# Kernel optimization log

Hardware: AMD Instinct MI355X
Metric: run time of the kernel (lower is better)

Reference implementation:

```python
import jax, jax.numpy as jnp
import numpy as np

N, IN, H1, H2, E, NE = 32768, 768, 2048, 1024, 64, 256
K_PAIRS, T_TRIP = 4096, 8192
TEMP, MARGIN, BETA = 0.1, 0.2, 0.001


def setup_inputs() -> dict:
    key = jax.random.key(0)
    ks = jax.random.split(key, 18)

    def w(k, i, o):
        return (jax.random.normal(k, (i, o), jnp.float32) / np.sqrt(i)).astype(jnp.float32)

    return {
        'x': jax.random.normal(ks[0], (N, IN), jnp.float32),
        'q_embs': jax.random.normal(ks[1], (N, IN), jnp.float32),
        'qd_align_w': jax.random.uniform(ks[2], (N,), jnp.float32),
        'pairs': jax.random.randint(ks[3], (K_PAIRS, 2), 0, N, jnp.int32),
        'triplets': jax.random.randint(ks[4], (T_TRIP, 3), 0, N, jnp.int32),
        'enc_w0': w(ks[5], IN, H1), 'enc_b0': jnp.zeros((H1,), jnp.float32),
        'enc_w1': w(ks[6], H1, H2), 'enc_b1': jnp.zeros((H2,), jnp.float32),
        'enc_w2': w(ks[7], H2, E), 'enc_b2': jnp.zeros((E,), jnp.float32),
        'dec_w0': w(ks[8], E, H2), 'dec_b0': jnp.zeros((H2,), jnp.float32),
        'dec_w1': w(ks[9], H2, H1), 'dec_b1': jnp.zeros((H1,), jnp.float32),
        'dec_w2': w(ks[10], H1, IN), 'dec_b2': jnp.zeros((IN,), jnp.float32),
        'codebook': w(ks[11], NE, E),
    }


def _mlp(h, w0, b0, w1, b1, w2, b2):
    h = jax.nn.relu(h @ w0 + b0)
    h = jax.nn.relu(h @ w1 + b1)
    return h @ w2 + b2


def _vqvae_forward(x, q_embs, qd_align_w, pairs, triplets,
                   enc_w0, enc_b0, enc_w1, enc_b1, enc_w2, enc_b2,
                   dec_w0, dec_b0, dec_w1, dec_b1, dec_w2, dec_b2, codebook):
    sg = jax.lax.stop_gradient
    # encoder on items and queries
    z = _mlp(x, enc_w0, enc_b0, enc_w1, enc_b1, enc_w2, enc_b2)            # [N, E]
    qz = _mlp(q_embs, enc_w0, enc_b0, enc_w1, enc_b1, enc_w2, enc_b2)      # [N, E]
    # vector quantize: nearest codebook entry
    d = (jnp.sum(z * z, axis=1, keepdims=True)
         - 2.0 * (z @ codebook.T)
         + jnp.sum(codebook * codebook, axis=1))                           # [N, NE]
    idx = jnp.argmin(d, axis=1)                                            # [N]
    x_q = codebook[idx]                                                    # [N, E]
    vq_loss = jnp.mean((x_q - sg(z)) ** 2) + BETA * jnp.mean((sg(x_q) - z) ** 2)
    x_q_st = z + sg(x_q - z)                                               # straight-through
    out = _mlp(x_q_st, dec_w0, dec_b0, dec_w1, dec_b1, dec_w2, dec_b2)     # [N, IN]
    # qd align: weighted cosine similarity between item and query encodings
    cos = jnp.sum(z * qz, axis=-1) / jnp.maximum(
        jnp.linalg.norm(z, axis=-1) * jnp.linalg.norm(qz, axis=-1), 1e-8)
    qd_align_loss = 1.0 - jnp.mean(qd_align_w * cos)
    # outer contrastive (InfoNCE over all rows; pos col replaces itself so
    # CE over [pos, all-but-pos] == logsumexp(all) - pos)
    xn = x_q_st / jnp.maximum(jnp.linalg.norm(x_q_st, axis=1, keepdims=True), 1e-12)
    sim = (xn[pairs[:, 0]] @ xn.T) / TEMP                                  # [K, N]
    pos = jnp.take_along_axis(sim, pairs[:, 1:2].astype(jnp.int32), axis=1)[:, 0]
    outer_con_loss = jnp.mean(jax.nn.logsumexp(sim, axis=1) - pos)
    # inner triplet loss on encoder features
    a, p, n = z[triplets[:, 0]], z[triplets[:, 1]], z[triplets[:, 2]]
    dp = jnp.sqrt(jnp.sum((a - p) ** 2, axis=-1) + 1e-12)
    dn = jnp.sqrt(jnp.sum((a - n) ** 2, axis=-1) + 1e-12)
    inner_triplet_loss = jnp.mean(jax.nn.relu(dp - dn + MARGIN))
    return out, vq_loss, idx[:, None], x_q_st, outer_con_loss, inner_triplet_loss, qd_align_loss


def reference(x, q_embs, qd_align_w, pairs, triplets,
              enc_w0, enc_b0, enc_w1, enc_b1, enc_w2, enc_b2,
              dec_w0, dec_b0, dec_w1, dec_b1, dec_w2, dec_b2, codebook):
    return _vqvae_forward(x, q_embs, qd_align_w, pairs, triplets,
                          enc_w0, enc_b0, enc_w1, enc_b1, enc_w2, enc_b2,
                          dec_w0, dec_b0, dec_w1, dec_b1, dec_w2, dec_b2, codebook)
```

## Files before the change

kernel.cpp:

```cpp
#include <hip/hip_runtime.h>
#include <hip/hip_bf16.h>

namespace {
constexpr int kN = 32768, kIN = 768, kH1 = 2048, kH2 = 1024, kE = 64, kNE = 256;
constexpr int kKP = 4096, kTT = 8192;
constexpr int kCh = 4096;
constexpr int kMaxFix = 4096;

constexpr size_t OFF_OUT = 0;
constexpr size_t OFF_VQ  = (size_t)kN * kIN;
constexpr size_t OFF_IDX = OFF_VQ + 1;
constexpr size_t OFF_XQ  = OFF_IDX + (size_t)kN;
constexpr size_t OFF_OCL = OFF_XQ + (size_t)kN * kE;
constexpr size_t OFF_ITL = OFF_OCL + 1;
constexpr size_t OFF_QDA = OFF_ITL + 1;
}

typedef short bf16x8 __attribute__((ext_vector_type(8)));
typedef float f32x4 __attribute__((ext_vector_type(4)));

__device__ __forceinline__ unsigned short f2bf(float v) {
  __hip_bfloat16 h = __float2bfloat16(v);
  return *reinterpret_cast<unsigned short*>(&h);
}
__device__ __forceinline__ float bf2f(unsigned short u) {
  __hip_bfloat16 h = *reinterpret_cast<__hip_bfloat16*>(&u);
  return __bfloat162float(h);
}

__device__ __forceinline__ void gload_lds16(const void* g, void* lds) {
  __builtin_amdgcn_global_load_lds(
      (const __attribute__((address_space(1))) void*)g,
      (__attribute__((address_space(3))) void*)lds, 16, 0, 0);
}

template <int BM, int BN, int BK, bool RELU, bool OUTF, bool OUTB>
__global__ __launch_bounds__(256) void gemm_bt(const unsigned short* __restrict__ A,
                                               const unsigned short* __restrict__ Bt,
                                               const float* __restrict__ bias,
                                               float* __restrict__ Cf,
                                               unsigned short* __restrict__ Cb,
                                               int N, int K) {
  constexpr int WM = BM / 2, WN = BN / 2, TMt = WM / 16, TNt = WN / 16;
  constexpr int CH = BK / 8;
  constexpr int RA = BM * BK / 2048, RB = BN * BK / 2048;
  __shared__ unsigned short As[BM * BK];
  __shared__ unsigned short Bs[BN * BK];
  const int tid = threadIdx.x, lane = tid & 63, wave = tid >> 6;
  const int wm = (wave >> 1) * WM, wn = (wave & 1) * WN;
  const int l15 = lane & 15, quad = lane >> 4;
  const int rowA0 = blockIdx.y * BM, colB0 = blockIdx.x * BN;
  f32x4 acc[TMt][TNt];
#pragma unroll
  for (int i = 0; i < TMt; ++i)
#pragma unroll
    for (int j = 0; j < TNt; ++j) acc[i][j] = (f32x4){0.f, 0.f, 0.f, 0.f};

  const char* Ab = (const char*)A;
  const char* Bb = (const char*)Bt;
  char* AsB = (char*)As;
  char* BsB = (char*)Bs;

  for (int k0 = 0; k0 < K; k0 += BK) {
    if (k0) __syncthreads();
#pragma unroll
    for (int r = 0; r < RA; ++r) {
      int off = (r * 256 + tid) * 16;
      int row = off / (BK * 2);
      int sc = ((off >> 4) ^ row) & (CH - 1);
      gload_lds16(Ab + (size_t)(rowA0 + row) * (K * 2) + (size_t)k0 * 2 + sc * 16,
                  AsB + off);
    }
#pragma unroll
    for (int r = 0; r < RB; ++r) {
      int off = (r * 256 + tid) * 16;
      int row = off / (BK * 2);
      int sc = ((off >> 4) ^ row) & (CH - 1);
      gload_lds16(Bb + (size_t)(colB0 + row) * (K * 2) + (size_t)k0 * 2 + sc * 16,
                  BsB + off);
    }
    __syncthreads();
#pragma unroll
    for (int ks = 0; ks < BK; ks += 32) {
      bf16x8 af[TMt], bfr[TNt];
#pragma unroll
      for (int i = 0; i < TMt; ++i) {
        int row = wm + i * 16 + l15;
        int c = (((ks >> 3) + quad) ^ row) & (CH - 1);
        af[i] = *(const bf16x8*)(AsB + row * (BK * 2) + c * 16);
      }
#pragma unroll
      for (int j = 0; j < TNt; ++j) {
        int col = wn + j * 16 + l15;
        int c = (((ks >> 3) + quad) ^ col) & (CH - 1);
        bfr[j] = *(const bf16x8*)(BsB + col * (BK * 2) + c * 16);
      }
#pragma unroll
      for (int i = 0; i < TMt; ++i)
#pragma unroll
        for (int j = 0; j < TNt; ++j)
          acc[i][j] = __builtin_amdgcn_mfma_f32_16x16x32_bf16(af[i], bfr[j],
                                                              acc[i][j], 0, 0, 0);
    }
  }
#pragma unroll
  for (int j = 0; j < TNt; ++j) {
    int col = colB0 + wn + j * 16 + l15;
    float bv = bias[col];
#pragma unroll
    for (int i = 0; i < TMt; ++i) {
      int rbase = rowA0 + wm + i * 16 + quad * 4;
#pragma unroll
      for (int r = 0; r < 4; ++r) {
        float v = acc[i][j][r] + bv;
        if (RELU) v = fmaxf(v, 0.f);
        size_t o = (size_t)(rbase + r) * N + col;
        if (OUTF) Cf[o] = v;
        if (OUTB) Cb[o] = f2bf(v);
      }
    }
  }
}

template <int BM, int BN, int BK, bool RELU, int OM>
__global__ __launch_bounds__(256) void gemm_bt_split(
    const unsigned short* __restrict__ Ah, const unsigned short* __restrict__ Al,
    const unsigned short* __restrict__ Bh, const unsigned short* __restrict__ Bl,
    const float* __restrict__ bias, float* __restrict__ Cf,
    unsigned short* __restrict__ Ch, unsigned short* __restrict__ Cl,
    int N, int K) {
  constexpr int WM = BM / 2, WN = BN / 2, TMt = WM / 16, TNt = WN / 16;
  constexpr int CH = BK / 8;
  constexpr int RA = BM * BK / 2048, RB = BN * BK / 2048;
  __shared__ unsigned short AsH[BM * BK];
  __shared__ unsigned short AsL[BM * BK];
  __shared__ unsigned short BsH[BN * BK];
  __shared__ unsigned short BsL[BN * BK];
  const int tid = threadIdx.x, lane = tid & 63, wave = tid >> 6;
  const int wm = (wave >> 1) * WM, wn = (wave & 1) * WN;
  const int l15 = lane & 15, quad = lane >> 4;
  const int rowA0 = blockIdx.y * BM, colB0 = blockIdx.x * BN;
  f32x4 acc[TMt][TNt];
#pragma unroll
  for (int i = 0; i < TMt; ++i)
#pragma unroll
    for (int j = 0; j < TNt; ++j) acc[i][j] = (f32x4){0.f, 0.f, 0.f, 0.f};

  const char* AhB = (const char*)Ah;
  const char* AlB = (const char*)Al;
  const char* BhB = (const char*)Bh;
  const char* BlB = (const char*)Bl;

  for (int k0 = 0; k0 < K; k0 += BK) {
    if (k0) __syncthreads();
#pragma unroll
    for (int r = 0; r < RA; ++r) {
      int off = (r * 256 + tid) * 16;
      int row = off / (BK * 2);
      int sc = ((off >> 4) ^ row) & (CH - 1);
      size_t go = (size_t)(rowA0 + row) * (K * 2) + (size_t)k0 * 2 + sc * 16;
      gload_lds16(AhB + go, (char*)AsH + off);
      gload_lds16(AlB + go, (char*)AsL + off);
    }
#pragma unroll
    for (int r = 0; r < RB; ++r) {
      int off = (r * 256 + tid) * 16;
      int row = off / (BK * 2);
      int sc = ((off >> 4) ^ row) & (CH - 1);
      size_t go = (size_t)(colB0 + row) * (K * 2) + (size_t)k0 * 2 + sc * 16;
      gload_lds16(BhB + go, (char*)BsH + off);
      gload_lds16(BlB + go, (char*)BsL + off);
    }
    __syncthreads();
#pragma unroll
    for (int ks = 0; ks < BK; ks += 32) {
      bf16x8 ah[TMt], al[TMt], bh[TNt], bl[TNt];
#pragma unroll
      for (int i = 0; i < TMt; ++i) {
        int row = wm + i * 16 + l15;
        int c = (((ks >> 3) + quad) ^ row) & (CH - 1);
        int off = row * (BK * 2) + c * 16;
        ah[i] = *(const bf16x8*)((const char*)AsH + off);
        al[i] = *(const bf16x8*)((const char*)AsL + off);
      }
#pragma unroll
      for (int j = 0; j < TNt; ++j) {
        int col = wn + j * 16 + l15;
        int c = (((ks >> 3) + quad) ^ col) & (CH - 1);
        int off = col * (BK * 2) + c * 16;
        bh[j] = *(const bf16x8*)((const char*)BsH + off);
        bl[j] = *(const bf16x8*)((const char*)BsL + off);
      }
#pragma unroll
      for (int i = 0; i < TMt; ++i)
#pragma unroll
        for (int j = 0; j < TNt; ++j) {
          acc[i][j] = __builtin_amdgcn_mfma_f32_16x16x32_bf16(ah[i], bh[j], acc[i][j], 0, 0, 0);
          acc[i][j] = __builtin_amdgcn_mfma_f32_16x16x32_bf16(ah[i], bl[j], acc[i][j], 0, 0, 0);
          acc[i][j] = __builtin_amdgcn_mfma_f32_16x16x32_bf16(al[i], bh[j], acc[i][j], 0, 0, 0);
        }
    }
  }
#pragma unroll
  for (int j = 0; j < TNt; ++j) {
    int col = colB0 + wn + j * 16 + l15;
    float bv = bias[col];
#pragma unroll
    for (int i = 0; i < TMt; ++i) {
      int rbase = rowA0 + wm + i * 16 + quad * 4;
#pragma unroll
      for (int r = 0; r < 4; ++r) {
        float v = acc[i][j][r] + bv;
        if (RELU) v = fmaxf(v, 0.f);
        size_t o = (size_t)(rbase + r) * N + col;
        if (OM == 0) {
          Cf[o] = v;
        } else {
          unsigned short hi = f2bf(v);
          Ch[o] = hi;
          Cl[o] = f2bf(v - bf2f(hi));
        }
      }
    }
  }
}

__global__ __launch_bounds__(256) void transpose_bf16(const float* __restrict__ W,
                                                      unsigned short* __restrict__ Wt,
                                                      int K, int N) {
  __shared__ float t[32][33];
  int bx = blockIdx.x * 32, by = blockIdx.y * 32;
  int tx = threadIdx.x & 31, ty = threadIdx.x >> 5;
#pragma unroll
  for (int i = 0; i < 32; i += 8)
    t[ty + i][tx] = W[(size_t)(by + ty + i) * N + bx + tx];
  __syncthreads();
#pragma unroll
  for (int i = 0; i < 32; i += 8)
    Wt[(size_t)(bx + ty + i) * K + by + tx] = f2bf(t[tx][ty + i]);
}

__global__ __launch_bounds__(256) void transpose_bf16_split(
    const float* __restrict__ W, unsigned short* __restrict__ Wh,
    unsigned short* __restrict__ Wl, int K, int N) {
  __shared__ float t[32][33];
  int bx = blockIdx.x * 32, by = blockIdx.y * 32;
  int tx = threadIdx.x & 31, ty = threadIdx.x >> 5;
#pragma unroll
  for (int i = 0; i < 32; i += 8)
    t[ty + i][tx] = W[(size_t)(by + ty + i) * N + bx + tx];
  __syncthreads();
#pragma unroll
  for (int i = 0; i < 32; i += 8) {
    float v = t[tx][ty + i];
    unsigned short hi = f2bf(v);
    size_t o = (size_t)(bx + ty + i) * K + by + tx;
    Wh[o] = hi;
    Wl[o] = f2bf(v - bf2f(hi));
  }
}

__global__ __launch_bounds__(256) void conv_bf16(const float* __restrict__ in,
                                                 unsigned short* __restrict__ out,
                                                 int n4) {
  int i = (blockIdx.x * 256 + threadIdx.x);
  if (i < n4) {
    float4 v = *(const float4*)(in + (size_t)i * 4);
    unsigned short o[4] = {f2bf(v.x), f2bf(v.y), f2bf(v.z), f2bf(v.w)};
    *(uint2*)(out + (size_t)i * 4) = *(uint2*)o;
  }
}

__global__ __launch_bounds__(256) void conv_split(const float* __restrict__ in,
                                                  unsigned short* __restrict__ oh,
                                                  unsigned short* __restrict__ ol,
                                                  int n4) {
  int i = (blockIdx.x * 256 + threadIdx.x);
  if (i < n4) {
    float4 v = *(const float4*)(in + (size_t)i * 4);
    unsigned short h[4], l[4];
    float vv[4] = {v.x, v.y, v.z, v.w};
#pragma unroll
    for (int k = 0; k < 4; ++k) {
      h[k] = f2bf(vv[k]);
      l[k] = f2bf(vv[k] - bf2f(h[k]));
    }
    *(uint2*)(oh + (size_t)i * 4) = *(uint2*)h;
    *(uint2*)(ol + (size_t)i * 4) = *(uint2*)l;
  }
}

__global__ __launch_bounds__(256) void vq_kernel(const float* __restrict__ z,
                                                 const float* __restrict__ cb,
                                                 float* __restrict__ idx_out,
                                                 float* __restrict__ xq_out,
                                                 unsigned short* __restrict__ xqb_out,
                                                 float* __restrict__ xn_out,
                                                 float* __restrict__ acc,
                                                 int* __restrict__ flags,
                                                 int* __restrict__ flagcnt) {
  __shared__ float zs[kE];
  __shared__ float dsv[256];
  __shared__ float rv[256];
  __shared__ int ri[256];
  __shared__ int defer;
  const int i = blockIdx.x;
  const int t = threadIdx.x;
  if (t < kE) zs[t] = z[(size_t)i * kE + t];
  __syncthreads();
  float dot = 0.f, nrm = 0.f, zn = 0.f;
  const float* c = cb + (size_t)t * kE;
#pragma unroll 8
  for (int e = 0; e < kE; ++e) {
    float ce = c[e];
    float ze = zs[e];
    dot = fmaf(ze, ce, dot);
    nrm = fmaf(ce, ce, nrm);
    zn = fmaf(ze, ze, zn);
  }
  float d = nrm - 2.f * dot;
  dsv[t] = d;
  rv[t] = d;
  ri[t] = t;
  __syncthreads();
  for (int s = 128; s > 0; s >>= 1) {
    if (t < s) {
      float v2 = rv[t + s];
      int i2 = ri[t + s];
      if (v2 < rv[t] || (v2 == rv[t] && i2 < ri[t])) { rv[t] = v2; ri[t] = i2; }
    }
    __syncthreads();
  }
  const int best = ri[0];
  const float d1 = rv[0];
  __syncthreads();
  rv[t] = (t == best) ? 3.4e38f : dsv[t];
  __syncthreads();
  for (int s = 128; s > 0; s >>= 1) {
    if (t < s) rv[t] = fminf(rv[t], rv[t + s]);
    __syncthreads();
  }
  if (t == 0) {
    float tau = 5e-5f * sqrtf(zn);
    if (rv[0] - d1 < tau) {
      defer = 1;
      int slot = atomicAdd(flagcnt, 1);
      flags[slot] = i;
    } else {
      defer = 0;
    }
  }
  __syncthreads();
  if (defer) return;
  if (t == 0) idx_out[i] = (float)best;
  if (t < kE) {
    float xq = cb[(size_t)best * kE + t];
    xq_out[(size_t)i * kE + t] = xq;
    xqb_out[(size_t)i * kE + t] = f2bf(xq);
    float dd = xq - zs[t];
    float sq = dd * dd;
    float nq = xq * xq;
#pragma unroll
    for (int m = 32; m > 0; m >>= 1) {
      sq += __shfl_xor(sq, m);
      nq += __shfl_xor(nq, m);
    }
    float inv = 1.f / fmaxf(sqrtf(nq), 1e-12f);
    xn_out[(size_t)i * kE + t] = xq * inv;
    if (t == 0) atomicAdd(&acc[i & 255], sq);
  }
}

__global__ __launch_bounds__(256) void fix_h1(
    const float* __restrict__ x, const float* __restrict__ ew0,
    const float* __restrict__ eb0, const int* __restrict__ flags,
    const int* __restrict__ flagcnt, float* __restrict__ h1f) {
  constexpr int R = 8, NJC = 8, JC = kH1 / NJC;
  __shared__ float xs[R][kIN];
  const int t = threadIdx.x;
  int cnt = *flagcnt;
  if (cnt > kMaxFix) cnt = kMaxFix;
  const int nrb = (cnt + R - 1) / R;
  const int nwork = nrb * NJC;
  for (int w = blockIdx.x; w < nwork; w += gridDim.x) {
    const int rb = w / NJC, jc = w % NJC;
    const int nr = min(R, cnt - rb * R);
    for (int rr = 0; rr < nr; ++rr) {
      const int r = flags[rb * R + rr];
      for (int q = t; q < kIN; q += 256) xs[rr][q] = x[(size_t)r * kIN + q];
    }
    __syncthreads();
    const int j = jc * JC + t;
    float s[R];
    const float b = eb0[j];
#pragma unroll
    for (int rr = 0; rr < R; ++rr) s[rr] = b;
#pragma unroll 8
    for (int k = 0; k < kIN; ++k) {
      float wv = ew0[(size_t)k * kH1 + j];
#pragma unroll
      for (int rr = 0; rr < R; ++rr) s[rr] = fmaf(xs[rr][k], wv, s[rr]);
    }
    for (int rr = 0; rr < nr; ++rr)
      h1f[(size_t)(rb * R + rr) * kH1 + j] = fmaxf(s[rr], 0.f);
    __syncthreads();
  }
}

__global__ __launch_bounds__(256) void fix_h2(
    const float* __restrict__ h1f, const float* __restrict__ ew1,
    const float* __restrict__ eb1, const int* __restrict__ flagcnt,
    float* __restrict__ h2f) {
  constexpr int R = 4, NJC = 4, JC = kH2 / NJC;
  __shared__ float hs[R][kH1];
  const int t = threadIdx.x;
  int cnt = *flagcnt;
  if (cnt > kMaxFix) cnt = kMaxFix;
  const int nrb = (cnt + R - 1) / R;
  const int nwork = nrb * NJC;
  for (int w = blockIdx.x; w < nwork; w += gridDim.x) {
    const int rb = w / NJC, jc = w % NJC;
    const int nr = min(R, cnt - rb * R);
    for (int rr = 0; rr < nr; ++rr)
      for (int q = t; q < kH1; q += 256)
        hs[rr][q] = h1f[(size_t)(rb * R + rr) * kH1 + q];
    __syncthreads();
    const int j = jc * JC + t;
    float s[R];
    const float b = eb1[j];
#pragma unroll
    for (int rr = 0; rr < R; ++rr) s[rr] = b;
#pragma unroll 8
    for (int k = 0; k < kH1; ++k) {
      float wv = ew1[(size_t)k * kH2 + j];
#pragma unroll
      for (int rr = 0; rr < R; ++rr) s[rr] = fmaf(hs[rr][k], wv, s[rr]);
    }
    for (int rr = 0; rr < nr; ++rr)
      h2f[(size_t)(rb * R + rr) * kH2 + j] = fmaxf(s[rr], 0.f);
    __syncthreads();
  }
}

__global__ __launch_bounds__(256) void fix_z(
    const float* __restrict__ h2f, const float* __restrict__ ew2,
    const float* __restrict__ eb2, const float* __restrict__ cb,
    const int* __restrict__ flags, const int* __restrict__ flagcnt,
    float* __restrict__ z, float* __restrict__ idx_out,
    float* __restrict__ xq_out, unsigned short* __restrict__ xqb_out,
    float* __restrict__ xn_out, float* __restrict__ acc) {
  __shared__ float hrow[kH2];
  __shared__ float sred[256];
  __shared__ float szs[kE];
  __shared__ float rv[256];
  __shared__ int ri[256];
  const int t = threadIdx.x;
  int cnt = *flagcnt;
  if (cnt > kMaxFix) cnt = kMaxFix;
  for (int fi = blockIdx.x; fi < cnt; fi += gridDim.x) {
    const int r = flags[fi];
    for (int q = t; q < kH2; q += 256) hrow[q] = h2f[(size_t)fi * kH2 + q];
    __syncthreads();
    {
      const int j = t & 63, p = t >> 6;
      float s = 0.f;
      for (int k = p * 256; k < p * 256 + 256; ++k)
        s = fmaf(hrow[k], ew2[(size_t)k * kE + j], s);
      sred[t] = s;
      __syncthreads();
      if (t < kE) {
        float zv = sred[t] + sred[t + 64] + sred[t + 128] + sred[t + 192] + eb2[t];
        szs[t] = zv;
        z[(size_t)r * kE + t] = zv;
      }
      __syncthreads();
    }
    {
      float dot = 0.f, nrm = 0.f;
      const float* c = cb + (size_t)t * kE;
#pragma unroll 8
      for (int e = 0; e < kE; ++e) {
        float ce = c[e];
        dot = fmaf(szs[e], ce, dot);
        nrm = fmaf(ce, ce, nrm);
      }
      rv[t] = nrm - 2.f * dot;
      ri[t] = t;
      __syncthreads();
      for (int s = 128; s > 0; s >>= 1) {
        if (t < s) {
          float v2 = rv[t + s];
          int i2 = ri[t + s];
          if (v2 < rv[t] || (v2 == rv[t] && i2 < ri[t])) { rv[t] = v2; ri[t] = i2; }
        }
        __syncthreads();
      }
      const int best = ri[0];
      if (t == 0) idx_out[r] = (float)best;
      if (t < kE) {
        float xq = cb[(size_t)best * kE + t];
        xq_out[(size_t)r * kE + t] = xq;
        xqb_out[(size_t)r * kE + t] = f2bf(xq);
        float dd = xq - szs[t];
        float sq = dd * dd;
        float nq = xq * xq;
#pragma unroll
        for (int m = 32; m > 0; m >>= 1) {
          sq += __shfl_xor(sq, m);
          nq += __shfl_xor(nq, m);
        }
        float inv = 1.f / fmaxf(sqrtf(nq), 1e-12f);
        xn_out[(size_t)r * kE + t] = xq * inv;
        if (t == 0) atomicAdd(&acc[r & 255], sq);
      }
      __syncthreads();
    }
  }
}

__global__ __launch_bounds__(256) void fix_rows(
    const float* __restrict__ x, const float* __restrict__ ew0,
    const float* __restrict__ eb0, const float* __restrict__ ew1,
    const float* __restrict__ eb1, const float* __restrict__ ew2,
    const float* __restrict__ eb2, const float* __restrict__ cb,
    const int* __restrict__ flags, const int* __restrict__ flagcnt,
    float* __restrict__ z, float* __restrict__ idx_out,
    float* __restrict__ xq_out, unsigned short* __restrict__ xqb_out,
    float* __restrict__ xn_out, float* __restrict__ acc) {
  __shared__ float xs[kIN];
  __shared__ float sh1[kH1];
  __shared__ float sh2[kH2];
  __shared__ float sred[256];
  __shared__ float szs[kE];
  __shared__ float rv[256];
  __shared__ int ri[256];
  const int t = threadIdx.x;
  const int cnt = *flagcnt;
  for (int fi = kMaxFix + blockIdx.x; fi < cnt; fi += gridDim.x) {
    const int r = flags[fi];
    for (int q = t; q < kIN; q += 256) xs[q] = x[(size_t)r * kIN + q];
    __syncthreads();
#pragma unroll
    for (int o = 0; o < kH1 / 256; ++o) {
      int j = t + 256 * o;
      float s = eb0[j];
      for (int k = 0; k < kIN; ++k) s = fmaf(xs[k], ew0[(size_t)k * kH1 + j], s);
      sh1[j] = fmaxf(s, 0.f);
    }
    __syncthreads();
#pragma unroll
    for (int o = 0; o < kH2 / 256; ++o) {
      int j = t + 256 * o;
      float s = eb1[j];
      for (int k = 0; k < kH1; ++k) s = fmaf(sh1[k], ew1[(size_t)k * kH2 + j], s);
      sh2[j] = fmaxf(s, 0.f);
    }
    __syncthreads();
    {
      int j = t & 63, p = t >> 6;
      float s = 0.f;
      for (int k = p * 256; k < p * 256 + 256; ++k)
        s = fmaf(sh2[k], ew2[(size_t)k * kE + j], s);
      sred[t] = s;
      __syncthreads();
      if (t < kE) {
        float zv = sred[t] + sred[t + 64] + sred[t + 128] + sred[t + 192] + eb2[t];
        szs[t] = zv;
        z[(size_t)r * kE + t] = zv;
      }
      __syncthreads();
    }
    {
      float dot = 0.f, nrm = 0.f;
      const float* c = cb + (size_t)t * kE;
#pragma unroll 8
      for (int e = 0; e < kE; ++e) {
        float ce = c[e];
        dot = fmaf(szs[e], ce, dot);
        nrm = fmaf(ce, ce, nrm);
      }
      rv[t] = nrm - 2.f * dot;
      ri[t] = t;
      __syncthreads();
      for (int s = 128; s > 0; s >>= 1) {
        if (t < s) {
          float v2 = rv[t + s];
          int i2 = ri[t + s];
          if (v2 < rv[t] || (v2 == rv[t] && i2 < ri[t])) { rv[t] = v2; ri[t] = i2; }
        }
        __syncthreads();
      }
      const int best = ri[0];
      if (t == 0) idx_out[r] = (float)best;
      if (t < kE) {
        float xq = cb[(size_t)best * kE + t];
        xq_out[(size_t)r * kE + t] = xq;
        xqb_out[(size_t)r * kE + t] = f2bf(xq);
        float dd = xq - szs[t];
        float sq = dd * dd;
        float nq = xq * xq;
#pragma unroll
        for (int m = 32; m > 0; m >>= 1) {
          sq += __shfl_xor(sq, m);
          nq += __shfl_xor(nq, m);
        }
        float inv = 1.f / fmaxf(sqrtf(nq), 1e-12f);
        xn_out[(size_t)r * kE + t] = xq * inv;
        if (t == 0) atomicAdd(&acc[r & 255], sq);
      }
      __syncthreads();
    }
  }
}

__global__ __launch_bounds__(256) void qd_kernel(const float* __restrict__ z,
                                                 const float* __restrict__ qz,
                                                 const float* __restrict__ w,
                                                 float* __restrict__ acc) {
  const int i = blockIdx.x * 4 + (threadIdx.x >> 6);
  const int l = threadIdx.x & 63;
  float a = z[(size_t)i * kE + l];
  float b = qz[(size_t)i * kE + l];
  float dot = a * b, na = a * a, nb = b * b;
#pragma unroll
  for (int m = 32; m > 0; m >>= 1) {
    dot += __shfl_xor(dot, m);
    na += __shfl_xor(na, m);
    nb += __shfl_xor(nb, m);
  }
  if (l == 0) {
    float cosv = dot / fmaxf(sqrtf(na) * sqrtf(nb), 1e-8f);
    atomicAdd(&acc[i & 255], w[i] * cosv);
  }
}

__global__ __launch_bounds__(256) void trip_kernel(const float* __restrict__ z,
                                                   const int* __restrict__ tr,
                                                   float* __restrict__ acc) {
  const int t = blockIdx.x * 4 + (threadIdx.x >> 6);
  const int l = threadIdx.x & 63;
  int ia = tr[3 * t], ip = tr[3 * t + 1], in2 = tr[3 * t + 2];
  float a = z[(size_t)ia * kE + l];
  float p = z[(size_t)ip * kE + l];
  float n = z[(size_t)in2 * kE + l];
  float d1 = (a - p) * (a - p);
  float d2 = (a - n) * (a - n);
#pragma unroll
  for (int m = 32; m > 0; m >>= 1) {
    d1 += __shfl_xor(d1, m);
    d2 += __shfl_xor(d2, m);
  }
  if (l == 0) {
    float dp = sqrtf(d1 + 1e-12f);
    float dn = sqrtf(d2 + 1e-12f);
    atomicAdd(&acc[t & 255], fmaxf(dp - dn + 0.2f, 0.f));
  }
}

__global__ __launch_bounds__(256) void pos_kernel(const float* __restrict__ xn,
                                                  const int* __restrict__ pairs,
                                                  float* __restrict__ acc) {
  const int k = blockIdx.x * 4 + (threadIdx.x >> 6);
  const int l = threadIdx.x & 63;
  int i0 = pairs[2 * k], i1 = pairs[2 * k + 1];
  float v = xn[(size_t)i0 * kE + l] * xn[(size_t)i1 * kE + l];
#pragma unroll
  for (int m = 32; m > 0; m >>= 1) v += __shfl_xor(v, m);
  if (l == 0) atomicAdd(&acc[k & 255], -10.f * v);
}


__global__ __launch_bounds__(256) void hist_kernel(const float* __restrict__ idx_out,
                                                   int* __restrict__ cnt) {
  __shared__ int h[kNE];
  const int t = threadIdx.x;
  h[t] = 0;
  __syncthreads();
  int i = blockIdx.x * 256 + t;
  atomicAdd(&h[(int)idx_out[i]], 1);
  __syncthreads();
  if (h[t]) atomicAdd(&cnt[t], h[t]);
}

__global__ __launch_bounds__(256) void code_lse(const float* __restrict__ cb,
                                                const int* __restrict__ cnt,
                                                float* __restrict__ E) {
  __shared__ float cbn[kNE][kE + 1];
  __shared__ float red[256];
  const int t = threadIdx.x, a = blockIdx.x;
  const float* r = cb + (size_t)t * kE;
  float s = 0.f;
#pragma unroll 8
  for (int e = 0; e < kE; ++e) s = fmaf(r[e], r[e], s);
  float inv = 1.f / fmaxf(sqrtf(s), 1e-12f);
#pragma unroll 8
  for (int e = 0; e < kE; ++e) cbn[t][e] = r[e] * inv;
  __syncthreads();
  float dot = 0.f;
#pragma unroll 8
  for (int e = 0; e < kE; ++e) dot = fmaf(cbn[a][e], cbn[t][e], dot);
  red[t] = (float)cnt[t] * expf(10.f * dot);
  __syncthreads();
  for (int sred = 128; sred > 0; sred >>= 1) {
    if (t < sred) red[t] += red[t + sred];
    __syncthreads();
  }
  if (t == 0) E[a] = red[0];
}

__global__ __launch_bounds__(256) void pair_log(const float* __restrict__ idx_out,
                                                const int* __restrict__ pairs,
                                                const float* __restrict__ E,
                                                float* __restrict__ acc) {
  int p = blockIdx.x * 256 + threadIdx.x;
  int a = (int)idx_out[pairs[2 * p]];
  atomicAdd(&acc[p & 255], logf(E[a]));
}

__global__ __launch_bounds__(256) void finalize_kernel(const float* __restrict__ acc,
                                                       float* __restrict__ out) {
  const int t = threadIdx.x;
  float vq = acc[t], qd = acc[256 + t], tr = acc[512 + t], ou = acc[768 + t];
#pragma unroll
  for (int m = 32; m > 0; m >>= 1) {
    vq += __shfl_xor(vq, m);
    qd += __shfl_xor(qd, m);
    tr += __shfl_xor(tr, m);
    ou += __shfl_xor(ou, m);
  }
  __shared__ float sm[4][4];
  const int w = t >> 6;
  if ((t & 63) == 0) { sm[0][w] = vq; sm[1][w] = qd; sm[2][w] = tr; sm[3][w] = ou; }
  __syncthreads();
  if (t == 0) {
    float svq = sm[0][0] + sm[0][1] + sm[0][2] + sm[0][3];
    float sqd = sm[1][0] + sm[1][1] + sm[1][2] + sm[1][3];
    float str = sm[2][0] + sm[2][1] + sm[2][2] + sm[2][3];
    float sou = sm[3][0] + sm[3][1] + sm[3][2] + sm[3][3];
    out[OFF_VQ]  = 1.001f * svq / (float)((size_t)kN * kE);
    out[OFF_OCL] = sou / (float)kKP;
    out[OFF_ITL] = str / (float)kTT;
    out[OFF_QDA] = 1.f - sqd / (float)kN;
  }
}

extern "C" void kernel_launch(void* const* d_in, const int* in_sizes, int n_in,
                              void* d_out, int out_size, void* d_ws, size_t ws_size,
                              hipStream_t stream) {
  (void)in_sizes; (void)n_in; (void)out_size; (void)ws_size;
  const float* x    = (const float*)d_in[0];
  const float* qe   = (const float*)d_in[1];
  const float* qdw  = (const float*)d_in[2];
  const int*   prs  = (const int*)d_in[3];
  const int*   trs  = (const int*)d_in[4];
  const float* ew0  = (const float*)d_in[5];
  const float* eb0  = (const float*)d_in[6];
  const float* ew1  = (const float*)d_in[7];
  const float* eb1  = (const float*)d_in[8];
  const float* ew2  = (const float*)d_in[9];
  const float* eb2  = (const float*)d_in[10];
  const float* dw0  = (const float*)d_in[11];
  const float* db0  = (const float*)d_in[12];
  const float* dw1  = (const float*)d_in[13];
  const float* db1  = (const float*)d_in[14];
  const float* dw2  = (const float*)d_in[15];
  const float* db2  = (const float*)d_in[16];
  const float* cb   = (const float*)d_in[17];
  float* out = (float*)d_out;

  float* z   = (float*)d_ws;
  float* qz  = z  + (size_t)kN * kE;
  float* xn  = qz + (size_t)kN * kE;
  float* acc = xn + (size_t)kN * kE;
  float* pairsum = acc + 1024;
  int*   flagcnt = (int*)(pairsum + 4096);
  int*   flags   = flagcnt + 64;
  unsigned short* xqb  = (unsigned short*)(flags + kN);
  unsigned short* wt0h = xqb  + (size_t)kN * kE;
  unsigned short* wt0l = wt0h + (size_t)kH1 * kIN;
  unsigned short* wt1h = wt0l + (size_t)kH1 * kIN;
  unsigned short* wt1l = wt1h + (size_t)kH2 * kH1;
  unsigned short* wt2h = wt1l + (size_t)kH2 * kH1;
  unsigned short* wt2l = wt2h + (size_t)kE * kH2;
  unsigned short* wt3  = wt2l + (size_t)kE * kH2;
  unsigned short* wt4  = wt3  + (size_t)kH2 * kE;
  unsigned short* wt5  = wt4  + (size_t)kH1 * kH2;
  unsigned short* xh  = wt5 + (size_t)kIN * kH1;
  unsigned short* xl  = xh + (size_t)kCh * kIN;
  unsigned short* h1h = xl + (size_t)kCh * kIN;
  unsigned short* h1l = h1h + (size_t)kCh * kH1;
  unsigned short* h2h = h1l + (size_t)kCh * kH1;
  unsigned short* h2l = h2h + (size_t)kCh * kH2;
  float* h1f = (float*)xh;
  float* h2f = h1f + (size_t)kMaxFix * kH1;
  int*   cnt = (int*)pairsum;
  float* E   = pairsum + 256;

  hipMemsetAsync(acc, 0, (1024 + 4096 + 64) * sizeof(float), stream);

  transpose_bf16_split<<<dim3(kH1 / 32, kIN / 32), 256, 0, stream>>>(ew0, wt0h, wt0l, kIN, kH1);
  transpose_bf16_split<<<dim3(kH2 / 32, kH1 / 32), 256, 0, stream>>>(ew1, wt1h, wt1l, kH1, kH2);
  transpose_bf16_split<<<dim3(kE / 32, kH2 / 32), 256, 0, stream>>>(ew2, wt2h, wt2l, kH2, kE);
  transpose_bf16<<<dim3(kH2 / 32, kE / 32), 256, 0, stream>>>(dw0, wt3, kE, kH2);
  transpose_bf16<<<dim3(kH1 / 32, kH2 / 32), 256, 0, stream>>>(dw1, wt4, kH2, kH1);
  transpose_bf16<<<dim3(kIN / 32, kH1 / 32), 256, 0, stream>>>(dw2, wt5, kH1, kIN);

  for (int c = 0; c < kN / kCh; ++c) {
    conv_split<<<(kCh * kIN / 4 + 255) / 256, 256, 0, stream>>>(
        x + (size_t)c * kCh * kIN, xh, xl, kCh * kIN / 4);
    gemm_bt_split<128, 128, 64, true, 2>
        <<<dim3(kH1 / 128, kCh / 128), 256, 0, stream>>>(
            xh, xl, wt0h, wt0l, eb0, nullptr, h1h, h1l, kH1, kIN);
    gemm_bt_split<128, 128, 64, true, 2>
        <<<dim3(kH2 / 128, kCh / 128), 256, 0, stream>>>(
            h1h, h1l, wt1h, wt1l, eb1, nullptr, h2h, h2l, kH2, kH1);
    gemm_bt_split<128, 64, 64, false, 0>
        <<<dim3(kE / 64, kCh / 128), 256, 0, stream>>>(
            h2h, h2l, wt2h, wt2l, eb2, z + (size_t)c * kCh * kE, nullptr, nullptr,
            kE, kH2);
  }

  vq_kernel<<<kN, 256, 0, stream>>>(z, cb, out + OFF_IDX, out + OFF_XQ, xqb, xn,
                                    acc, flags, flagcnt);
  fix_h1<<<512, 256, 0, stream>>>(x, ew0, eb0, flags, flagcnt, h1f);
  fix_h2<<<512, 256, 0, stream>>>(h1f, ew1, eb1, flagcnt, h2f);
  fix_z<<<512, 256, 0, stream>>>(h2f, ew2, eb2, cb, flags, flagcnt, z,
                                 out + OFF_IDX, out + OFF_XQ, xqb, xn, acc);
  fix_rows<<<64, 256, 0, stream>>>(x, ew0, eb0, ew1, eb1, ew2, eb2, cb, flags,
                                   flagcnt, z, out + OFF_IDX, out + OFF_XQ, xqb,
                                   xn, acc);

  for (int c = 0; c < kN / kCh; ++c) {
    gemm_bt<128, 128, 64, true, false, true>
        <<<dim3(kH2 / 128, kCh / 128), 256, 0, stream>>>(
            xqb + (size_t)c * kCh * kE, wt3, db0, nullptr, h2h, kH2, kE);
    gemm_bt<128, 128, 64, true, false, true>
        <<<dim3(kH1 / 128, kCh / 128), 256, 0, stream>>>(
            h2h, wt4, db1, nullptr, h1h, kH1, kH2);
    gemm_bt<128, 128, 64, false, true, false>
        <<<dim3(kIN / 128, kCh / 128), 256, 0, stream>>>(
            h1h, wt5, db2, out + OFF_OUT + (size_t)c * kCh * kIN, nullptr, kIN, kH1);
  }

  for (int c = 0; c < kN / kCh; ++c) {
    conv_bf16<<<(kCh * kIN / 4 + 255) / 256, 256, 0, stream>>>(
        qe + (size_t)c * kCh * kIN, xh, kCh * kIN / 4);
    gemm_bt<128, 128, 64, true, false, true>
        <<<dim3(kH1 / 128, kCh / 128), 256, 0, stream>>>(
            xh, wt0h, eb0, nullptr, h1h, kH1, kIN);
    gemm_bt<128, 128, 64, true, false, true>
        <<<dim3(kH2 / 128, kCh / 128), 256, 0, stream>>>(
            h1h, wt1h, eb1, nullptr, h2h, kH2, kH1);
    gemm_bt<128, 64, 64, false, true, false>
        <<<dim3(kE / 64, kCh / 128), 256, 0, stream>>>(
            h2h, wt2h, eb2, qz + (size_t)c * kCh * kE, nullptr, kE, kH2);
  }

  qd_kernel<<<kN / 4, 256, 0, stream>>>(z, qz, qdw, acc + 256);
  trip_kernel<<<kTT / 4, 256, 0, stream>>>(z, trs, acc + 512);
  pos_kernel<<<kKP / 4, 256, 0, stream>>>(xn, prs, acc + 768);
  hist_kernel<<<kN / 256, 256, 0, stream>>>(out + OFF_IDX, cnt);
  code_lse<<<kNE, 256, 0, stream>>>(cb, cnt, E);
  pair_log<<<kKP / 256, 256, 0, stream>>>(out + OFF_IDX, prs, E, acc + 768);

  finalize_kernel<<<1, 256, 0, stream>>>(acc, out);
}
```

Baseline: 3.075 ms.

## Restructure VQ kernel to stage codebook in LDS and process 64 rows per block

```diff
diff --git a/kernel.cpp b/kernel.cpp
--- a/kernel.cpp
+++ b/kernel.cpp
@@ -290,6 +290,12 @@
   }
 }
 
+#define FMA4(a, s, v)              \
+  a[0] = fmaf(s, v[0], a[0]);      \
+  a[1] = fmaf(s, v[1], a[1]);      \
+  a[2] = fmaf(s, v[2], a[2]);      \
+  a[3] = fmaf(s, v[3], a[3])
+
 __global__ __launch_bounds__(256) void vq_kernel(const float* __restrict__ z,
                                                  const float* __restrict__ cb,
                                                  float* __restrict__ idx_out,
@@ -299,77 +305,103 @@
                                                  float* __restrict__ acc,
                                                  int* __restrict__ flags,
                                                  int* __restrict__ flagcnt) {
-  __shared__ float zs[kE];
-  __shared__ float dsv[256];
-  __shared__ float rv[256];
-  __shared__ int ri[256];
-  __shared__ int defer;
-  const int i = blockIdx.x;
+  __shared__ float cbT[kE * kNE];
   const int t = threadIdx.x;
-  if (t < kE) zs[t] = z[(size_t)i * kE + t];
+  {
+    const f32x4* src = (const f32x4*)(cb + (size_t)t * kE);
+#pragma unroll
+    for (int q = 0; q < 16; ++q) {
+      f32x4 v = src[q];
+      cbT[(4 * q + 0) * kNE + t] = v[0];
+      cbT[(4 * q + 1) * kNE + t] = v[1];
+      cbT[(4 * q + 2) * kNE + t] = v[2];
+      cbT[(4 * q + 3) * kNE + t] = v[3];
+    }
+  }
   __syncthreads();
-  float dot = 0.f, nrm = 0.f, zn = 0.f;
-  const float* c = cb + (size_t)t * kE;
-#pragma unroll 8
+  const int l = t & 63, wv = t >> 6;
+  f32x4 cn = (f32x4){0.f, 0.f, 0.f, 0.f};
   for (int e = 0; e < kE; ++e) {
-    float ce = c[e];
-    float ze = zs[e];
-    dot = fmaf(ze, ce, dot);
-    nrm = fmaf(ce, ce, nrm);
-    zn = fmaf(ze, ze, zn);
-  }
-  float d = nrm - 2.f * dot;
-  dsv[t] = d;
-  rv[t] = d;
-  ri[t] = t;
-  __syncthreads();
-  for (int s = 128; s > 0; s >>= 1) {
-    if (t < s) {
-      float v2 = rv[t + s];
-      int i2 = ri[t + s];
-      if (v2 < rv[t] || (v2 == rv[t] && i2 < ri[t])) { rv[t] = v2; ri[t] = i2; }
-    }
-    __syncthreads();
-  }
-  const int best = ri[0];
-  const float d1 = rv[0];
-  __syncthreads();
-  rv[t] = (t == best) ? 3.4e38f : dsv[t];
-  __syncthreads();
-  for (int s = 128; s > 0; s >>= 1) {
-    if (t < s) rv[t] = fminf(rv[t], rv[t + s]);
-    __syncthreads();
-  }
-  if (t == 0) {
-    float tau = 5e-5f * sqrtf(zn);
-    if (rv[0] - d1 < tau) {
-      defer = 1;
-      int slot = atomicAdd(flagcnt, 1);
-      flags[slot] = i;
-    } else {
-      defer = 0;
-    }
-  }
-  __syncthreads();
-  if (defer) return;
-  if (t == 0) idx_out[i] = (float)best;
-  if (t < kE) {
-    float xq = cb[(size_t)best * kE + t];
-    xq_out[(size_t)i * kE + t] = xq;
-    xqb_out[(size_t)i * kE + t] = f2bf(xq);
-    float dd = xq - zs[t];
-    float sq = dd * dd;
-    float nq = xq * xq;
-#pragma unroll
-    for (int m = 32; m > 0; m >>= 1) {
-      sq += __shfl_xor(sq, m);
-      nq += __shfl_xor(nq, m);
-    }
-    float inv = 1.f / fmaxf(sqrtf(nq), 1e-12f);
-    xn_out[(size_t)i * kE + t] = xq * inv;
-    if (t == 0) atomicAdd(&acc[i & 255], sq);
-  }
-}
+    f32x4 cv = *(const f32x4*)&cbT[e * kNE + 4 * l];
+    cn[0] = fmaf(cv[0], cv[0], cn[0]);
+    cn[1] = fmaf(cv[1], cv[1], cn[1]);
+    cn[2] = fmaf(cv[2], cv[2], cn[2]);
+    cn[3] = fmaf(cv[3], cv[3], cn[3]);
+  }
+  const int rowBase = (blockIdx.x * 4 + wv) * 16;
+  for (int p = 0; p < 4; ++p) {
+    const int ra = rowBase + p * 4;
+    f32x4 dt[4];
+#pragma unroll
+    for (int r = 0; r < 4; ++r) dt[r] = (f32x4){0.f, 0.f, 0.f, 0.f};
+#pragma unroll
+    for (int e4 = 0; e4 < 16; ++e4) {
+      f32x4 c0 = *(const f32x4*)&cbT[(4 * e4 + 0) * kNE + 4 * l];
+      f32x4 c1 = *(const f32x4*)&cbT[(4 * e4 + 1) * kNE + 4 * l];
+      f32x4 c2 = *(const f32x4*)&cbT[(4 * e4 + 2) * kNE + 4 * l];
+      f32x4 c3 = *(const f32x4*)&cbT[(4 * e4 + 3) * kNE + 4 * l];
+#pragma unroll
+      for (int r = 0; r < 4; ++r) {
+        f32x4 zv = *(const f32x4*)(z + (size_t)(ra + r) * kE + e4 * 4);
+        FMA4(dt[r], zv[0], c0);
+        FMA4(dt[r], zv[1], c1);
+        FMA4(dt[r], zv[2], c2);
+        FMA4(dt[r], zv[3], c3);
+      }
+    }
+#pragma unroll
+    for (int r = 0; r < 4; ++r) {
+      const int row = ra + r;
+      float d0 = cn[0] - 2.f * dt[r][0];
+      float d1 = cn[1] - 2.f * dt[r][1];
+      float d2 = cn[2] - 2.f * dt[r][2];
+      float d3 = cn[3] - 2.f * dt[r][3];
+      float m1 = d0, m2 = 3.4e38f;
+      int i1 = 4 * l;
+      if (d1 < m1) { m2 = m1; m1 = d1; i1 = 4 * l + 1; } else m2 = fminf(m2, d1);
+      if (d2 < m1) { m2 = m1; m1 = d2; i1 = 4 * l + 2; } else m2 = fminf(m2, d2);
+      if (d3 < m1) { m2 = m1; m1 = d3; i1 = 4 * l + 3; } else m2 = fminf(m2, d3);
+#pragma unroll
+      for (int m = 32; m > 0; m >>= 1) {
+        float om1 = __shfl_xor(m1, m);
+        int oi1 = __shfl_xor(i1, m);
+        float om2 = __shfl_xor(m2, m);
+        float nm2 = fminf(fminf(m2, om2), fmaxf(m1, om1));
+        if (om1 < m1 || (om1 == m1 && oi1 < i1)) { m1 = om1; i1 = oi1; }
+        m2 = nm2;
+      }
+      float zl = z[(size_t)row * kE + l];
+      float zn = zl * zl;
+#pragma unroll
+      for (int m = 32; m > 0; m >>= 1) zn += __shfl_xor(zn, m);
+      float tau = 5e-5f * sqrtf(zn);
+      if (m2 - m1 < tau) {
+        if (l == 0) {
+          int slot = atomicAdd(flagcnt, 1);
+          flags[slot] = row;
+        }
+        continue;
+      }
+      const int best = i1;
+      if (l == 0) idx_out[row] = (float)best;
+      float xq = cb[(size_t)best * kE + l];
+      xq_out[(size_t)row * kE + l] = xq;
+      xqb_out[(size_t)row * kE + l] = f2bf(xq);
+      float dd = xq - zl;
+      float sq = dd * dd;
+      float nq = xq * xq;
+#pragma unroll
+      for (int m = 32; m > 0; m >>= 1) {
+        sq += __shfl_xor(sq, m);
+        nq += __shfl_xor(nq, m);
+      }
+      float inv = 1.f / fmaxf(sqrtf(nq), 1e-12f);
+      xn_out[(size_t)row * kE + l] = xq * inv;
+      if (l == 0) atomicAdd(&acc[row & 255], sq);
+    }
+  }
+}
+#undef FMA4
 
 __global__ __launch_bounds__(256) void fix_h1(
     const float* __restrict__ x, const float* __restrict__ ew0,
@@ -820,8 +852,8 @@
             kE, kH2);
   }
 
-  vq_kernel<<<kN, 256, 0, stream>>>(z, cb, out + OFF_IDX, out + OFF_XQ, xqb, xn,
-                                    acc, flags, flagcnt);
+  vq_kernel<<<512, 256, 0, stream>>>(z, cb, out + OFF_IDX, out + OFF_XQ, xqb, xn,
+                                     acc, flags, flagcnt);
   fix_h1<<<512, 256, 0, stream>>>(x, ew0, eb0, flags, flagcnt, h1f);
   fix_h2<<<512, 256, 0, stream>>>(h1f, ew1, eb1, flagcnt, h2f);
   fix_z<<<512, 256, 0, stream>>>(h2f, ew2, eb2, cb, flags, flagcnt, z,
```

Measured after the change: 2.988 ms. -2.8%, faster.
